# Optimization experiments

Hardware: AMD Instinct MI355X
Metric: run time of the kernel (lower is better)

The kernel has to match this reference:

```python
import jax, jax.numpy as jnp
import numpy as np

BLOCK, HALO, HEADS, DH = 8, 4, 4, 32
EPS = 1e-5


def _convT(x, w, p):
    # torch ConvTranspose2d(stride=1, padding=p) == conv with flipped/transposed kernel, padding k-1-p
    k = w.shape[-1]
    w2 = jnp.flip(w, axis=(-2, -1)).transpose(1, 0, 2, 3)  # (Cin,Cout,k,k) -> (Cout,Cin,k,k)
    pad = k - 1 - p
    return jax.lax.conv_general_dilated(x, w2, (1, 1), ((pad, pad), (pad, pad)),
                                        dimension_numbers=('NCHW', 'OIHW', 'NCHW'))


def _bn(x, g, b, m, v):
    s = g * jax.lax.rsqrt(v + EPS)
    return x * s[None, :, None, None] + (b - m * s)[None, :, None, None]


def _rel_to_abs(x):
    # x: [b, l, 2r-1] -> [b, l, r]
    b, l, m = x.shape
    r = (m + 1) // 2
    x = jnp.concatenate([x, jnp.zeros((b, l, 1), x.dtype)], axis=2)
    flat = jnp.concatenate([x.reshape(b, l * (m + 1)), jnp.zeros((b, m - l), x.dtype)], axis=1)
    return flat.reshape(b, l + 1, m)[:, :l, -r:]


def _rel_logits_1d(q, rel_k):
    # q: [b, x, y, d]; rel_k: [2r-1, d] -> [b, x, r, y, r]
    b, x, y, d = q.shape
    r = (rel_k.shape[0] + 1) // 2
    logits = jnp.einsum('bxyd,rd->bxyr', q, rel_k)
    logits = _rel_to_abs(logits.reshape(b * x, y, -1)).reshape(b, x, y, r)
    return jnp.broadcast_to(logits[:, :, None, :, :], (b, x, r, y, r))


def _rel_pos_emb(q, rel_h, rel_w):
    # q: [bb, block*block, dh] (already scaled, per halonet-pytorch)
    bb, n, d = q.shape
    qg = q.reshape(bb, BLOCK, BLOCK, d)
    lw = _rel_logits_1d(qg, rel_w).transpose(0, 1, 3, 2, 4).reshape(bb, n, -1)  # b (x y) (i j)
    lh = _rel_logits_1d(qg.transpose(0, 2, 1, 3), rel_h).transpose(0, 3, 1, 4, 2).reshape(bb, n, -1)  # b (y x) (j i)
    return lw + lh


def _halo_attn(x, to_q, to_kv, to_out_w, to_out_b, rel_h, rel_w):
    B, C, H, W = x.shape
    b, h = BLOCK, HALO
    nh, nw = H // b, W // b
    nblk = nh * nw
    wsz = b + 2 * h
    inner = to_q.shape[1]
    scale = DH ** -0.5
    # queries: non-overlapping blocks -> [B*nblk, b*b, C]
    q_inp = x.reshape(B, C, nh, b, nw, b).transpose(0, 2, 4, 3, 5, 1).reshape(B * nblk, b * b, C)
    # keys/values: overlapping halo windows (F.unfold) -> [B*nblk, wsz*wsz, C]
    pat = jax.lax.conv_general_dilated_patches(x, (wsz, wsz), (b, b), ((h, h), (h, h)))  # [B, C*wsz*wsz, nh, nw]
    kv_inp = pat.reshape(B, C, wsz * wsz, nblk).transpose(0, 3, 2, 1).reshape(B * nblk, wsz * wsz, C)
    q = q_inp @ to_q
    k, v = jnp.split(kv_inp @ to_kv, 2, axis=-1)
    def heads(t):
        return t.reshape(t.shape[0], t.shape[1], HEADS, DH).transpose(0, 2, 1, 3).reshape(-1, t.shape[1], DH)
    q, k, v = heads(q) * scale, heads(k), heads(v)
    sim = jnp.einsum('bid,bjd->bij', q, k) + _rel_pos_emb(q, rel_h, rel_w)  # [B*nblk*HEADS, b*b, wsz*wsz]
    # mask out halo positions that fall into zero padding
    ones = jnp.ones((1, 1, H, W), x.dtype)
    mpat = jax.lax.conv_general_dilated_patches(ones, (wsz, wsz), (b, b), ((h, h), (h, h)))
    mask = mpat.reshape(wsz * wsz, nblk).T > 0  # [nblk, wsz*wsz]
    neg = -jnp.finfo(sim.dtype).max
    sim = jnp.where(mask[None, :, None, None, :],
                    sim.reshape(B, nblk, HEADS, b * b, wsz * wsz), neg)
    attn = jax.nn.softmax(sim, axis=-1).reshape(-1, b * b, wsz * wsz)
    out = jnp.einsum('bij,bjd->bid', attn, v)
    out = out.reshape(B * nblk, HEADS, b * b, DH).transpose(0, 2, 1, 3).reshape(B * nblk, b * b, inner)
    out = out @ to_out_w + to_out_b
    return out.reshape(B, nh, nw, b, b, C).transpose(0, 5, 1, 3, 2, 4).reshape(B, C, H, W)


def setup_inputs() -> dict:
    key = jax.random.key(0)
    ks = jax.random.split(key, 13)
    B, C, H, W = 2, 128, 192, 192
    inner = HEADS * DH
    rel = 2 * (BLOCK + 2 * HALO) - 1  # 31
    n = lambda k, s, sc: jax.random.normal(k, s, jnp.float32) * sc
    return {
        'x': jax.random.normal(ks[0], (B, C, H, W), jnp.float32),
        'conv1_w': n(ks[1], (C, C, 1, 1), 0.1),
        'bn1_g': jnp.ones((C,), jnp.float32), 'bn1_b': jnp.zeros((C,), jnp.float32),
        'bn1_m': n(ks[2], (C,), 0.1),
        'bn1_v': jax.random.uniform(ks[3], (C,), jnp.float32, 0.5, 1.5),
        'to_q': n(ks[4], (C, inner), 0.05), 'to_kv': n(ks[5], (C, 2 * inner), 0.05),
        'to_out_w': n(ks[6], (inner, C), 0.05), 'to_out_b': n(ks[7], (C,), 0.01),
        'rel_h': n(ks[8], (rel, DH), DH ** -0.5), 'rel_w': n(ks[9], (rel, DH), DH ** -0.5),
        'conv3_w': n(ks[10], (C, C, 3, 3), 0.05),
        'bn3_g': jnp.ones((C,), jnp.float32), 'bn3_b': jnp.zeros((C,), jnp.float32),
        'bn3_m': n(ks[11], (C,), 0.1),
        'bn3_v': jax.random.uniform(ks[12], (C,), jnp.float32, 0.5, 1.5),
    }


def reference(x, conv1_w, bn1_g, bn1_b, bn1_m, bn1_v, to_q, to_kv, to_out_w, to_out_b,
              rel_h, rel_w, conv3_w, bn3_g, bn3_b, bn3_m, bn3_v):
    # Bottleneck (stride=1, no downsample): conv1x1T -> BN -> ReLU -> HaloAttention -> ReLU
    #   -> conv3x3T -> BN -> +identity -> ReLU
    out = jax.nn.relu(_bn(_convT(x, conv1_w, 0), bn1_g, bn1_b, bn1_m, bn1_v))
    out = jax.nn.relu(_halo_attn(out, to_q, to_kv, to_out_w, to_out_b, rel_h, rel_w))
    out = _bn(_convT(out, conv3_w, 1), bn3_g, bn3_b, bn3_m, bn3_v)
    return jax.nn.relu(out + x)
```

## Files before the change

kernel.cpp:

```cpp
#include <hip/hip_runtime.h>
#include <hip/hip_bf16.h>

using bf16 = __hip_bfloat16;
typedef unsigned short u16;
typedef unsigned int   u32;
typedef __attribute__((ext_vector_type(8))) short short8;
typedef __attribute__((ext_vector_type(4))) float f32x4;

#define B_N 2
#define CCH 128
#define HH 192
#define WW 192
#define HWS (HH*WW)
#define NBLKS 576
#define EPSV 1e-5f
#define LDW 136

__device__ __forceinline__ float b2f(bf16 v){ return __bfloat162float(v); }
__device__ __forceinline__ bf16  f2b(float v){ return __float2bfloat16(v); }
__device__ __forceinline__ u32 pck(float a, float b){
    bf16 x = f2b(a), y = f2b(b);
    return (u32)*(u16*)&x | ((u32)*(u16*)&y << 16);
}

__global__ __launch_bounds__(256) void prep_w(
    const float* __restrict__ w1, const float* __restrict__ to_q,
    const float* __restrict__ to_kv, const float* __restrict__ to_ow,
    const float* __restrict__ w3, const float* __restrict__ relh,
    const float* __restrict__ relw, bf16* __restrict__ wb)
{
    int i = blockIdx.x*256 + threadIdx.x;
    float v;
    if (i < 16384){       int co=(i>>7)&127, ci=i&127;      v = w1[ci*128+co]; }
    else if (i < 32768){  int r=i-16384; int co=r>>7, ci=r&127; v = to_q[ci*128+co]*0.17677669529663687f; }
    else if (i < 49152){  int r=i-32768; int co=r>>7, ci=r&127; v = to_kv[ci*256+co]; }
    else if (i < 65536){  int r=i-49152; int co=r>>7, ci=r&127; v = to_kv[ci*256+128+co]; }
    else if (i < 81920){  int r=i-65536; int co=r>>7, ci=r&127; v = to_ow[ci*128+co]; }
    else if (i < 229376){ int r=i-81920; int tap=r>>14, co=(r>>7)&127, ci=r&127; int a=tap/3, b=tap-a*3;
                          v = w3[((size_t)(ci*128+co)*3+a)*3+b]; }
    else if (i < 230400){ int j=i-229376; v = (j < 992) ? relh[j] : 0.f; }
    else                { int j=i-230400; v = (j < 992) ? relw[j] : 0.f; }
    wb[i] = f2b(v);
}

__global__ __launch_bounds__(256) void conv1_mfma(
    const float* __restrict__ x, const bf16* __restrict__ Wp,
    bf16* __restrict__ outp,
    const float* __restrict__ bn_g, const float* __restrict__ bn_b,
    const float* __restrict__ bn_m, const float* __restrict__ bn_v)
{
    __shared__ float tF[128*68];
    __shared__ u16   sX[64*LDW];
    u16* sW = (u16*)tF;
    const int tid  = threadIdx.x;
    const int pix0 = blockIdx.x * 64;
    const int n    = pix0 / HWS;
    const int hwb  = pix0 - n*HWS;
    const int lane = tid & 63;
    const int ln = lane & 15, g = lane >> 4;
    const int cow = (tid >> 6) * 32;

    #pragma unroll
    for (int r = 0; r < 8; ++r){
        int e = tid + r*256;
        int ci = e >> 4, p4 = e & 15;
        *(float4*)&tF[ci*68 + p4*4] =
            *(const float4*)&x[(size_t)(n*CCH + ci)*HWS + hwb + p4*4];
    }
    __syncthreads();
    {
        const int pix = tid & 63, cq = tid >> 6;
        u32 pkt[16];
        #pragma unroll
        for (int c = 0; c < 16; ++c){
            int ci = cq*32 + c*2;
            pkt[c] = pck(tF[ci*68 + pix], tF[(ci+1)*68 + pix]);
        }
        u32* dst = (u32*)&sX[pix*LDW + cq*32];
        #pragma unroll
        for (int c = 0; c < 16; ++c) dst[c] = pkt[c];
    }
    __syncthreads();
    #pragma unroll
    for (int r = 0; r < 8; ++r){
        int e = tid + r*256; int row = e>>4, grp = e&15;
        *(uint4*)&sW[row*LDW + grp*8] = *(const uint4*)&Wp[row*128 + grp*8];
    }
    __syncthreads();

    f32x4 acc[4][2];
    #pragma unroll
    for (int mi=0;mi<4;mi++)
        #pragma unroll
        for (int ni=0;ni<2;ni++) acc[mi][ni] = (f32x4){0.f,0.f,0.f,0.f};
    #pragma unroll
    for (int kk = 0; kk < 4; ++kk){
        short8 fa[4], fb[2];
        #pragma unroll
        for (int mi=0;mi<4;mi++)
            fa[mi] = *(const short8*)&sX[(mi*16+ln)*LDW + kk*32 + g*8];
        #pragma unroll
        for (int ni=0;ni<2;ni++)
            fb[ni] = *(const short8*)&sW[(cow+ni*16+ln)*LDW + kk*32 + g*8];
        #pragma unroll
        for (int mi=0;mi<4;mi++)
            #pragma unroll
            for (int ni=0;ni<2;ni++)
                acc[mi][ni] = __builtin_amdgcn_mfma_f32_16x16x32_bf16(fa[mi], fb[ni], acc[mi][ni], 0, 0, 0);
    }
    float sc[2], bb[2];
    #pragma unroll
    for (int ni=0;ni<2;ni++){
        int co = cow + ni*16 + ln;
        float sg = bn_g[co]*rsqrtf(bn_v[co]+EPSV);
        sc[ni] = sg; bb[ni] = bn_b[co] - bn_m[co]*sg;
    }
    #pragma unroll
    for (int mi=0;mi<4;mi++)
        #pragma unroll
        for (int ni=0;ni<2;ni++)
            #pragma unroll
            for (int j=0;j<4;j++){
                int pix = pix0 + mi*16 + g*4 + j;
                int co  = cow + ni*16 + ln;
                float v = fmaxf(acc[mi][ni][j]*sc[ni] + bb[ni], 0.f);
                outp[(size_t)pix*CCH + co] = f2b(v);
            }
}

template<bool DO_BIAS, bool DO_RELU, bool TRANS_Y2>
__global__ __launch_bounds__(256) void gemm_mfma(
    const bf16* __restrict__ inp, const bf16* __restrict__ Wp,
    bf16* __restrict__ outp, bf16* __restrict__ outp2, int cstride, int choff,
    const float* __restrict__ bias)
{
    Wp    += (size_t)blockIdx.y * 16384;
    choff += blockIdx.y * 128;
    __shared__ u16 sW[128*LDW];
    __shared__ u16 sX[64*LDW];
    const int tid  = threadIdx.x;
    const int pix0 = blockIdx.x * 64;
    const int lane = tid & 63;
    const int ln = lane & 15, g = lane >> 4;
    const int cow = (tid >> 6) * 32;

    #pragma unroll
    for (int r = 0; r < 8; ++r){
        int e = tid + r*256; int row = e>>4, grp = e&15;
        *(uint4*)&sW[row*LDW + grp*8] = *(const uint4*)&Wp[row*128 + grp*8];
    }
    #pragma unroll
    for (int r = 0; r < 4; ++r){
        int e = tid + r*256; int row = e>>4, grp = e&15;
        *(uint4*)&sX[row*LDW + grp*8] = *(const uint4*)&inp[(size_t)(pix0+row)*CCH + grp*8];
    }
    __syncthreads();

    f32x4 acc[4][2];
    #pragma unroll
    for (int mi=0;mi<4;mi++)
        #pragma unroll
        for (int ni=0;ni<2;ni++) acc[mi][ni] = (f32x4){0.f,0.f,0.f,0.f};

    #pragma unroll
    for (int kk = 0; kk < 4; ++kk){
        short8 fa[4], fb[2];
        #pragma unroll
        for (int mi=0;mi<4;mi++)
            fa[mi] = *(const short8*)&sX[(mi*16+ln)*LDW + kk*32 + g*8];
        #pragma unroll
        for (int ni=0;ni<2;ni++)
            fb[ni] = *(const short8*)&sW[(cow+ni*16+ln)*LDW + kk*32 + g*8];
        #pragma unroll
        for (int mi=0;mi<4;mi++)
            #pragma unroll
            for (int ni=0;ni<2;ni++)
                acc[mi][ni] = __builtin_amdgcn_mfma_f32_16x16x32_bf16(fa[mi], fb[ni], acc[mi][ni], 0, 0, 0);
    }

    if (TRANS_Y2 && blockIdx.y == 2){
        __syncthreads();
        u16* tile = sX;
        #pragma unroll
        for (int mi=0;mi<4;mi++)
            #pragma unroll
            for (int ni=0;ni<2;ni++){
                int co   = cow + ni*16 + ln;
                int pixl = mi*16 + g*4;
                *(u32*)&tile[co*68 + pixl]     = pck(acc[mi][ni][0], acc[mi][ni][1]);
                *(u32*)&tile[co*68 + pixl + 2] = pck(acc[mi][ni][2], acc[mi][ni][3]);
            }
        __syncthreads();
        const int co2 = tid >> 1, hf = tid & 1;
        const int n2 = pix0 / HWS, hwb2 = pix0 - n2*HWS;
        u16* gdst = (u16*)outp2 + (size_t)(n2*CCH + co2)*HWS + hwb2 + hf*32;
        const u16* src = &tile[co2*68 + hf*32];
        #pragma unroll
        for (int k=0;k<8;k++)
            *(uint2*)&gdst[k*4] = *(const uint2*)&src[k*4];
        return;
    }

    float bb[2];
    #pragma unroll
    for (int ni=0;ni<2;ni++){
        int co = cow + ni*16 + ln;
        bb[ni] = DO_BIAS ? bias[co] : 0.f;
    }
    #pragma unroll
    for (int mi=0;mi<4;mi++)
        #pragma unroll
        for (int ni=0;ni<2;ni++)
            #pragma unroll
            for (int j=0;j<4;j++){
                int pix = pix0 + mi*16 + g*4 + j;
                int co  = cow + ni*16 + ln;
                float v = acc[mi][ni][j] + bb[ni];
                if (DO_RELU) v = fmaxf(v, 0.f);
                outp[(size_t)pix*cstride + choff + co] = f2b(v);
            }
}

__global__ __launch_bounds__(256) void conv3_mfma(
    const bf16* __restrict__ inp, const bf16* __restrict__ W3p,
    const float* __restrict__ xin, float* __restrict__ outp,
    const float* __restrict__ g3, const float* __restrict__ b3,
    const float* __restrict__ m3, const float* __restrict__ v3)
{
    __shared__ u16 sW[128*LDW];
    __shared__ u16 sX[64*LDW];
    const int tid = threadIdx.x;
    const int P0  = blockIdx.x * 64;
    const int n   = P0 / HWS;
    const int hwb = P0 - n*HWS;
    const int h = hwb / WW, wb = hwb - h*WW;
    const int lane = tid & 63, ln = lane & 15, g = lane >> 4;
    const int cow = (tid >> 6) * 32;

    f32x4 acc[2][4];
    #pragma unroll
    for (int mi=0;mi<2;mi++)
        #pragma unroll
        for (int ni=0;ni<4;ni++) acc[mi][ni] = (f32x4){0.f,0.f,0.f,0.f};

    for (int tap = 0; tap < 9; ++tap){
        const int a = tap/3, b = tap - a*3;
        const int hs = h + 1 - a;
        if (hs < 0 || hs >= HH) continue;
        const int ws0 = wb + 1 - b;
        __syncthreads();
        #pragma unroll
        for (int r = 0; r < 8; ++r){
            int e = tid + r*256; int row = e>>4, grp = e&15;
            *(uint4*)&sW[row*LDW + grp*8] = *(const uint4*)&W3p[tap*16384 + row*128 + grp*8];
        }
        #pragma unroll
        for (int r = 0; r < 4; ++r){
            int e = tid + r*256; int row = e>>4, grp = e&15;
            int wsrc = ws0 + row;
            uint4 val = {0u,0u,0u,0u};
            if (wsrc >= 0 && wsrc < WW)
                val = *(const uint4*)&inp[(size_t)(n*HWS + hs*WW + wsrc)*CCH + grp*8];
            *(uint4*)&sX[row*LDW + grp*8] = val;
        }
        __syncthreads();
        #pragma unroll
        for (int kk = 0; kk < 4; ++kk){
            short8 fa[2], fb[4];
            #pragma unroll
            for (int mi=0;mi<2;mi++)
                fa[mi] = *(const short8*)&sW[(cow+mi*16+ln)*LDW + kk*32 + g*8];
            #pragma unroll
            for (int ni=0;ni<4;ni++)
                fb[ni] = *(const short8*)&sX[(ni*16+ln)*LDW + kk*32 + g*8];
            #pragma unroll
            for (int mi=0;mi<2;mi++)
                #pragma unroll
                for (int ni=0;ni<4;ni++)
                    acc[mi][ni] = __builtin_amdgcn_mfma_f32_16x16x32_bf16(fa[mi], fb[ni], acc[mi][ni], 0, 0, 0);
        }
    }

    #pragma unroll
    for (int mi=0;mi<2;mi++)
        #pragma unroll
        for (int j=0;j<4;j++){
            int co = cow + mi*16 + g*4 + j;
            float sg = g3[co]*rsqrtf(v3[co]+EPSV);
            float bc = b3[co] - m3[co]*sg;
            #pragma unroll
            for (int ni=0;ni<4;ni++){
                int pixl = hwb + ni*16 + ln;
                size_t idx = (size_t)(n*CCH + co)*HWS + pixl;
                float v = acc[mi][ni][j]*sg + bc + xin[idx];
                outp[idx] = fmaxf(v, 0.f);
            }
        }
}

__global__ __launch_bounds__(512) void attn_kernel(
    const u16* __restrict__ QK, const u16* __restrict__ vT,
    const u16* __restrict__ relb, bf16* __restrict__ outp)
{
    __shared__ __align__(16) char smem[46848];
    u16*   sK   = (u16*)(smem);
    u16*   sP   = (u16*)(smem);
    u16*   sVT  = (u16*)(smem + 20480);
    float* tT   = (float*)(smem + 37376);
    float* wredM= (float*)(smem + 45824);
    float* wredS= (float*)(smem + 46336);

    const int tid  = threadIdx.x;
    const int bid0 = blockIdx.x;
    const int bid  = (bid0 & 7) * 576 + (bid0 >> 3);
    const int head = bid & 3;
    const int t    = bid >> 2;
    const int n    = t / NBLKS;
    const int blk  = t - n*NBLKS;
    const int bi = blk / 24, bj = blk - bi*24;
    const int row0 = bi*8 - 4, col0 = bj*8 - 4;
    const int ch0 = head*32;
    const int wv = tid >> 6, lane = tid & 63, ln = lane & 15, g = lane >> 4;
    const int nt = wv & 3, mh = wv >> 2;

    uint2 vreg[4];
    #pragma unroll
    for (int r = 0; r < 4; ++r){
        int e = tid + r*512;
        int d   = e >> 6;
        int rem = e & 63;
        int iw  = rem >> 2;
        int jc  = (rem & 3) * 4;
        int rr  = row0 + iw, cc0 = col0 + jc;
        uint2 vv = {0u,0u};
        if (rr >= 0 && rr < HH && cc0 >= 0 && cc0 < 189)
            vv = *(const uint2*)&vT[(size_t)(n*CCH + ch0 + d)*HWS + rr*WW + cc0];
        vreg[r] = vv;
    }

    #pragma unroll
    for (int r = 0; r < 2; ++r){
        int e = tid + r*512;
        int wp = e >> 2, q4 = e & 3;
        int rr = row0 + (wp>>4), cc2 = col0 + (wp&15);
        uint4 kk4 = {0u,0u,0u,0u};
        if (rr>=0 && rr<HH && cc2>=0 && cc2<WW){
            size_t P = (size_t)n*HWS + rr*WW + cc2;
            kk4 = *(const uint4*)&QK[P*256 + 128 + ch0 + q4*8];
        }
        *(uint4*)&sK[wp*40 + q4*8] = kk4;
    }

    const int qc = nt*16 + ln;
    size_t Pq = (size_t)n*HWS + (bi*8 + (qc>>3))*WW + bj*8 + (qc&7);
    const short8 qfrag = *(const short8*)&QK[Pq*256 + ch0 + g*8];
    __syncthreads();

    f32x4 accs[8];
    #pragma unroll
    for (int i=0;i<8;i++){
        short8 fk = *(const short8*)&sK[((mh*8+i)*16+ln)*40 + g*8];
        accs[i] = __builtin_amdgcn_mfma_f32_16x16x32_bf16(fk, qfrag, (f32x4){0.f,0.f,0.f,0.f}, 0, 0, 0);
    }

    {
        const u16* relX = relb + (mh ? 1024 : 0);
        #pragma unroll
        for (int ntr=0; ntr<2; ++ntr){
            short8 fr = *(const short8*)&relX[(ntr*16+ln)*32 + g*8];
            f32x4 L = __builtin_amdgcn_mfma_f32_16x16x32_bf16(qfrag, fr, (f32x4){0.f,0.f,0.f,0.f}, 0, 0, 0);
            #pragma unroll
            for (int r2=0;r2<4;r2++){
                int q  = nt*16 + g*4 + r2;
                int rr = ntr*16 + ln;
                int bq = mh ? (q&7) : (q>>3);
                int iw = rr - 15 + bq;
                if (iw >= 0 && iw < 16) tT[mh*1056 + iw*66 + q] = L[r2];
            }
        }
    }
    __syncthreads();

    float tw[4];
    bool cok[4];
    #pragma unroll
    for (int r2=0;r2<4;r2++){
        tw[r2] = tT[1056 + (g*4+r2)*66 + qc];
        int cc2 = col0 + g*4 + r2;
        cok[r2] = (cc2 >= 0 && cc2 < WW);
    }
    float mx = -3.4e38f;
    #pragma unroll
    for (int i=0;i<8;i++){
        int mt = mh*8 + i;
        int rr = row0 + mt;
        bool rok = (rr >= 0 && rr < HH);
        float th = tT[mt*66 + qc];
        #pragma unroll
        for (int r2=0;r2<4;r2++){
            float s = (rok && cok[r2]) ? (accs[i][r2] + th + tw[r2]) : -3.0e38f;
            accs[i][r2] = s;
            mx = fmaxf(mx, s);
        }
    }
    mx = fmaxf(mx, __shfl_xor(mx, 16));
    mx = fmaxf(mx, __shfl_xor(mx, 32));
    if (g == 0) wredM[mh*64 + qc] = mx;
    __syncthreads();

    #pragma unroll
    for (int r = 0; r < 4; ++r){
        int e = tid + r*512;
        int d   = e >> 6;
        int rem = e & 63;
        int iw  = rem >> 2;
        int jc  = (rem & 3) * 4;
        *(uint2*)&sVT[d*264 + iw*16 + jc] = vreg[r];
    }
    mx = fmaxf(wredM[qc], wredM[64 + qc]);

    float sm = 0.f;
    #pragma unroll
    for (int i=0;i<8;i++){
        #pragma unroll
        for (int r2=0;r2<4;r2++){
            float p = __expf(accs[i][r2] - mx);
            accs[i][r2] = p;
            sm += p;
        }
    }
    sm += __shfl_xor(sm, 16);
    sm += __shfl_xor(sm, 32);
    if (g == 0) wredS[mh*64 + qc] = sm;
    if (mh == 0){
        #pragma unroll
        for (int i=0;i<8;i++){
            u32* dst = (u32*)&sP[qc*136 + i*16 + g*4];
            dst[0] = pck(accs[i][0], accs[i][1]);
            dst[1] = pck(accs[i][2], accs[i][3]);
        }
    }
    __syncthreads();

    const int dt = wv & 1, qt = wv >> 1;
    f32x4 acco = (f32x4){0.f,0.f,0.f,0.f};
    #pragma unroll
    for (int ks=0; ks<4; ++ks){
        short8 fa = *(const short8*)&sVT[(dt*16+ln)*264 + ks*32 + g*8];
        short8 fb = *(const short8*)&sP [(qt*16+ln)*136 + ks*32 + g*8];
        acco = __builtin_amdgcn_mfma_f32_16x16x32_bf16(fa, fb, acco, 0, 0, 0);
    }
    __syncthreads();
    if (mh == 1){
        #pragma unroll
        for (int i=0;i<8;i++){
            u32* dst = (u32*)&sP[qc*136 + i*16 + g*4];
            dst[0] = pck(accs[i][0], accs[i][1]);
            dst[1] = pck(accs[i][2], accs[i][3]);
        }
    }
    __syncthreads();

    #pragma unroll
    for (int ks=0; ks<4; ++ks){
        short8 fa = *(const short8*)&sVT[(dt*16+ln)*264 + 128 + ks*32 + g*8];
        short8 fb = *(const short8*)&sP [(qt*16+ln)*136 + ks*32 + g*8];
        acco = __builtin_amdgcn_mfma_f32_16x16x32_bf16(fa, fb, acco, 0, 0, 0);
    }
    {
        const int q = qt*16 + ln;
        const float inv = 1.f / (wredS[q] + wredS[64 + q]);
        size_t P = (size_t)n*HWS + (bi*8 + (q>>3))*WW + bj*8 + (q&7);
        uint2 ov;
        ov.x = pck(acco[0]*inv, acco[1]*inv);
        ov.y = pck(acco[2]*inv, acco[3]*inv);
        *(uint2*)&outp[P*CCH + ch0 + dt*16 + g*4] = ov;
    }
}

extern "C" void kernel_launch(void* const* d_in, const int* in_sizes, int n_in,
                              void* d_out, int out_size, void* d_ws, size_t ws_size,
                              hipStream_t stream)
{
    (void)in_sizes; (void)n_in; (void)out_size; (void)ws_size;
    const float* x      = (const float*)d_in[0];
    const float* w1     = (const float*)d_in[1];
    const float* bn1_g  = (const float*)d_in[2];
    const float* bn1_b  = (const float*)d_in[3];
    const float* bn1_m  = (const float*)d_in[4];
    const float* bn1_v  = (const float*)d_in[5];
    const float* to_q   = (const float*)d_in[6];
    const float* to_kv  = (const float*)d_in[7];
    const float* to_ow  = (const float*)d_in[8];
    const float* to_ob  = (const float*)d_in[9];
    const float* rel_h  = (const float*)d_in[10];
    const float* rel_w  = (const float*)d_in[11];
    const float* w3     = (const float*)d_in[12];
    const float* bn3_g  = (const float*)d_in[13];
    const float* bn3_b  = (const float*)d_in[14];
    const float* bn3_m  = (const float*)d_in[15];
    const float* bn3_v  = (const float*)d_in[16];

    char* ws   = (char*)d_ws;
    bf16* out1 = (bf16*)(ws + 0);
    bf16* qk   = (bf16*)(ws + 18874368);
    bf16* vT   = (bf16*)(ws + 75497472);
    bf16* wb   = (bf16*)(ws + 94371840);
    bf16* W3p  = wb + 81920;
    u16*  relb = (u16*)(wb + 229376);
    bf16* attnout = (bf16*)d_out;
    bf16* out2    = out1;

    prep_w<<<904, 256, 0, stream>>>(w1, to_q, to_kv, to_ow, w3, rel_h, rel_w, wb);

    conv1_mfma<<<1152, 256, 0, stream>>>(x, wb, out1, bn1_g, bn1_b, bn1_m, bn1_v);
    gemm_mfma<false,false,true><<<dim3(1152,3), 256, 0, stream>>>(
        out1, wb + 16384, qk, vT, 256, 0, nullptr);

    attn_kernel<<<4608, 512, 0, stream>>>((const u16*)qk, (const u16*)vT,
                                          relb, attnout);

    gemm_mfma<true,true,false><<<dim3(1152,1), 256, 0, stream>>>(
        attnout, wb + 65536, out2, nullptr, 128, 0, to_ob);

    conv3_mfma<<<1152, 256, 0, stream>>>(out2, W3p, x, (float*)d_out,
                                         bn3_g, bn3_b, bn3_m, bn3_v);
}
```

Before: 159.2 us.

## Reuse halo row tile across horizontal taps and read conv3 weights from global

The conv3 kernel now stages one input row segment of 66 pixels with a halo in shared memory per kernel row and reuses it for all three horizontal taps by offsetting the read index. This replaces staging a 64-pixel tile per tap. Weights are no longer copied into shared memory and are read straight from global memory (through cache) as MFMA operands. The aim is fewer barriers and less LDS traffic and footprint, which should help occupancy. The cost is uncoalesced per-lane global weight loads in the inner loop, whose latency may not be hidden.

```diff
diff --git a/kernel.cpp b/kernel.cpp
--- a/kernel.cpp
+++ b/kernel.cpp
@@ -227,8 +227,7 @@
     const float* __restrict__ g3, const float* __restrict__ b3,
     const float* __restrict__ m3, const float* __restrict__ v3)
 {
-    __shared__ u16 sW[128*LDW];
-    __shared__ u16 sX[64*LDW];
+    __shared__ u16 sXh[66*136];
     const int tid = threadIdx.x;
     const int P0  = blockIdx.x * 64;
     const int n   = P0 / HWS;
@@ -243,41 +242,41 @@
         #pragma unroll
         for (int ni=0;ni<4;ni++) acc[mi][ni] = (f32x4){0.f,0.f,0.f,0.f};
 
-    for (int tap = 0; tap < 9; ++tap){
-        const int a = tap/3, b = tap - a*3;
+    for (int a = 0; a < 3; ++a){
         const int hs = h + 1 - a;
         if (hs < 0 || hs >= HH) continue;
-        const int ws0 = wb + 1 - b;
         __syncthreads();
         #pragma unroll
-        for (int r = 0; r < 8; ++r){
-            int e = tid + r*256; int row = e>>4, grp = e&15;
-            *(uint4*)&sW[row*LDW + grp*8] = *(const uint4*)&W3p[tap*16384 + row*128 + grp*8];
-        }
-        #pragma unroll
-        for (int r = 0; r < 4; ++r){
-            int e = tid + r*256; int row = e>>4, grp = e&15;
-            int wsrc = ws0 + row;
-            uint4 val = {0u,0u,0u,0u};
-            if (wsrc >= 0 && wsrc < WW)
-                val = *(const uint4*)&inp[(size_t)(n*HWS + hs*WW + wsrc)*CCH + grp*8];
-            *(uint4*)&sX[row*LDW + grp*8] = val;
+        for (int r = 0; r < 5; ++r){
+            int e = tid + r*256;
+            if (e < 1056){
+                int cs = e >> 4, grp = e & 15;
+                int col = wb - 1 + cs;
+                uint4 val = {0u,0u,0u,0u};
+                if (col >= 0 && col < WW)
+                    val = *(const uint4*)&inp[(size_t)(n*HWS + hs*WW + col)*CCH + grp*8];
+                *(uint4*)&sXh[cs*136 + grp*8] = val;
+            }
         }
         __syncthreads();
-        #pragma unroll
-        for (int kk = 0; kk < 4; ++kk){
-            short8 fa[2], fb[4];
-            #pragma unroll
-            for (int mi=0;mi<2;mi++)
-                fa[mi] = *(const short8*)&sW[(cow+mi*16+ln)*LDW + kk*32 + g*8];
-            #pragma unroll
-            for (int ni=0;ni<4;ni++)
-                fb[ni] = *(const short8*)&sX[(ni*16+ln)*LDW + kk*32 + g*8];
-            #pragma unroll
-            for (int mi=0;mi<2;mi++)
+        for (int b = 0; b < 3; ++b){
+            const int tap = a*3 + b;
+            const bf16* Wt = W3p + tap*16384;
+            #pragma unroll
+            for (int kk = 0; kk < 4; ++kk){
+                short8 fa[2], fb[4];
+                #pragma unroll
+                for (int mi=0;mi<2;mi++)
+                    fa[mi] = *(const short8*)&Wt[(cow+mi*16+ln)*128 + kk*32 + g*8];
                 #pragma unroll
                 for (int ni=0;ni<4;ni++)
-                    acc[mi][ni] = __builtin_amdgcn_mfma_f32_16x16x32_bf16(fa[mi], fb[ni], acc[mi][ni], 0, 0, 0);
+                    fb[ni] = *(const short8*)&sXh[(ni*16+ln + 2 - b)*136 + kk*32 + g*8];
+                #pragma unroll
+                for (int mi=0;mi<2;mi++)
+                    #pragma unroll
+                    for (int ni=0;ni<4;ni++)
+                        acc[mi][ni] = __builtin_amdgcn_mfma_f32_16x16x32_bf16(fa[mi], fb[ni], acc[mi][ni], 0, 0, 0);
+            }
         }
     }
 
```

Result: slower. 176.5 us (+10.9%).
